# Performance work log

Hardware: AMD Instinct MI355X
Metric: run time of the kernel (lower is better)

Reference implementation:

```python
import jax, jax.numpy as jnp
import numpy as np

N_NODES = 50000
N_EDGES = 800000
IN_CH, HID_CH, OUT_CH = 256, 128, 64


def setup_inputs() -> dict:
    key = jax.random.key(0)
    k_x, k_e, k_w1, k_w2 = jax.random.split(key, 4)
    x = jax.random.normal(k_x, (N_NODES, IN_CH), dtype=jnp.float32)
    edge_index = jax.random.randint(k_e, (2, N_EDGES), 0, N_NODES, dtype=jnp.int32)
    # Glorot-style init like PyG GCNConv (weight [in, out], bias zeros)
    s1 = float(np.sqrt(6.0 / (IN_CH + HID_CH)))
    s2 = float(np.sqrt(6.0 / (HID_CH + OUT_CH)))
    W1 = jax.random.uniform(k_w1, (IN_CH, HID_CH), jnp.float32, -s1, s1)
    b1 = jnp.zeros((HID_CH,), jnp.float32)
    W2 = jax.random.uniform(k_w2, (HID_CH, OUT_CH), jnp.float32, -s2, s2)
    b2 = jnp.zeros((OUT_CH,), jnp.float32)
    return {"x": x, "edge_index": edge_index, "W1": W1, "b1": b1, "W2": W2, "b2": b2}


def _gcn_conv(x, src, dst, deg_inv_sqrt, W, b, n_nodes):
    """GCNConv with self-loops: D^{-1/2}(A+I)D^{-1/2} X W + b."""
    h = x @ W  # [N, out]
    norm = deg_inv_sqrt[src] * deg_inv_sqrt[dst]          # [E]
    msgs = h[src] * norm[:, None]                          # [E, out] gather
    agg = jax.ops.segment_sum(msgs, dst, num_segments=n_nodes)  # scatter-add
    self_loop = h * (deg_inv_sqrt * deg_inv_sqrt)[:, None]      # self-loop term
    return agg + self_loop + b


def reference(x, edge_index, W1, b1, W2, b2):
    n = x.shape[0]
    src, dst = edge_index[0], edge_index[1]
    # degree includes self-loop (+1), edge weight 1, counted at destination
    deg = jnp.zeros((n,), x.dtype).at[dst].add(1.0) + 1.0
    dis = jax.lax.rsqrt(deg)
    h = jax.nn.relu(_gcn_conv(x, src, dst, dis, W1, b1, n))
    out = jax.nn.relu(_gcn_conv(h, src, dst, dis, W2, b2, n))
    return out
```

## Files before the change

### kernel.cpp

```cpp
#include <hip/hip_runtime.h>

#define N_NODES 50000
#define N_EDGES 800000
#define IN_CH 256
#define HID_CH 128
#define OUT_CH 64
#define CAP 64
#define NBINS 196
#define PCHUNK 3200
#define PBLOCKS 250
#define SWZ_ELEMS (IN_CH * HID_CH + HID_CH * OUT_CH)
#define SWZ_BLOCKS (SWZ_ELEMS / 256)

typedef _Float16 f16;
typedef _Float16 f16x8 __attribute__((ext_vector_type(8)));
typedef float f32x4 __attribute__((ext_vector_type(4)));
typedef unsigned short u16;
typedef unsigned int u32;

template <int K, int N>
__device__ __forceinline__ void swz(const float* __restrict__ W, f16* __restrict__ Bsw,
                                    int idx) {
    constexpr int NTILES = N / 16;
    int j = idx & 7;
    int lane = (idx >> 3) & 63;
    int rest = idx >> 9;
    int nt = rest % NTILES;
    int ks = rest / NTILES;
    int k = ks * 32 + (lane >> 4) * 8 + j;
    int n = nt * 16 + (lane & 15);
    Bsw[idx] = (f16)W[(size_t)k * N + n];
}

__device__ __forceinline__ void scan_local(const int* __restrict__ binCnt,
                                           int* sc, int* vv) {
    const int t = threadIdx.x;
    int v = (t < NBINS) ? binCnt[t] : 0;
    sc[t] = v; vv[t] = v;
    __syncthreads();
    for (int ofs = 1; ofs < 256; ofs <<= 1) {
        int add = (t >= ofs) ? sc[t - ofs] : 0;
        __syncthreads();
        sc[t] += add;
        __syncthreads();
    }
}

__global__ __launch_bounds__(256) void k_pre(const int* __restrict__ dst,
                                             int* __restrict__ binCnt,
                                             const float* __restrict__ W1,
                                             const float* __restrict__ W2,
                                             f16* __restrict__ B1,
                                             f16* __restrict__ B2) {
    if ((int)blockIdx.x < PBLOCKS) {
        __shared__ int lcnt[NBINS];
        for (int i = threadIdx.x; i < NBINS; i += 256) lcnt[i] = 0;
        __syncthreads();
        int base = blockIdx.x * PCHUNK;
        for (int i = base + (int)threadIdx.x; i < base + PCHUNK; i += 256)
            atomicAdd(&lcnt[dst[i] >> 8], 1);
        __syncthreads();
        for (int i = threadIdx.x; i < NBINS; i += 256)
            if (lcnt[i]) atomicAdd(&binCnt[i], lcnt[i]);
        return;
    }
    int idx = ((int)blockIdx.x - PBLOCKS) * 256 + threadIdx.x;
    if (idx < IN_CH * HID_CH) {
        swz<IN_CH, HID_CH>(W1, B1, idx);
    } else {
        idx -= IN_CH * HID_CH;
        if (idx < HID_CH * OUT_CH) swz<HID_CH, OUT_CH>(W2, B2, idx);
    }
}

__global__ __launch_bounds__(256) void k_place(const int* __restrict__ src,
                                               const int* __restrict__ dst,
                                               const int* __restrict__ binCnt,
                                               int* __restrict__ binCursor,
                                               u32* __restrict__ ebuf, int E) {
    __shared__ u32 codes[PCHUNK];
    __shared__ int sc[256], vv[256];
    __shared__ int lcnt[NBINS], lbase[NBINS], lcur[NBINS];
    scan_local(binCnt, sc, vv);
    for (int i = threadIdx.x; i < NBINS; i += 256) lcnt[i] = 0;
    __syncthreads();
    int base = blockIdx.x * PCHUNK;
    int m = min(PCHUNK, E - base);
    for (int j = threadIdx.x; j < m; j += 256) {
        u32 d = (u32)dst[base + j];
        codes[j] = (d << 16) | (u32)src[base + j];
        atomicAdd(&lcnt[d >> 8], 1);
    }
    __syncthreads();
    for (int i = threadIdx.x; i < NBINS; i += 256) {
        lbase[i] = (sc[i] - vv[i]) + atomicAdd(&binCursor[i], lcnt[i]);
        lcur[i] = 0;
    }
    __syncthreads();
    for (int j = threadIdx.x; j < m; j += 256) {
        u32 c = codes[j];
        int b = c >> 24;
        int p = atomicAdd(&lcur[b], 1);
        ebuf[lbase[b] + p] = c;
    }
}

__global__ __launch_bounds__(256) void k_build(const u32* __restrict__ ebuf,
                                               const int* __restrict__ binCnt,
                                               int* __restrict__ cnt,
                                               float* __restrict__ dis,
                                               u16* __restrict__ bucket, int N) {
    __shared__ int sc[256], vv[256];
    __shared__ int lcnt[256];
    __shared__ u16 lbuck[256 * CAP];
    scan_local(binCnt, sc, vv);
    int t = threadIdx.x;
    lcnt[t] = 0;
    __syncthreads();
    int b = blockIdx.x;
    int s = sc[b] - vv[b];
    int e = sc[b];
    for (int i = s + t; i < e; i += 256) {
        u32 c = ebuf[i];
        int local = (c >> 16) & 255;
        int p = atomicAdd(&lcnt[local], 1);
        if (p < CAP) lbuck[local * CAP + p] = (u16)(c & 0xFFFFu);
    }
    __syncthreads();
    int nodeBase = b << 8;
    if (nodeBase + t < N) {
        cnt[nodeBase + t] = lcnt[t];
        dis[nodeBase + t] = rsqrtf((float)lcnt[t] + 1.0f);
    }
    const uint4* lsrc = (const uint4*)lbuck;
    uint4* gdst = (uint4*)(bucket + (size_t)nodeBase * CAP);
    for (int idx = t; idx < 256 * CAP / 8; idx += 256) {
        int row = idx >> 3;
        int chunk = idx & 7;
        if (nodeBase + row < N && (chunk << 3) < lcnt[row]) gdst[idx] = lsrc[idx];
    }
}

template <int K, int N, bool A_FP32, bool RELU>
__global__ __launch_bounds__(256) void k_gemm(const void* __restrict__ Av,
                                              const f16* __restrict__ Bsw,
                                              const float* __restrict__ dis,
                                              f16* __restrict__ C, int M) {
    constexpr int KSTEPS = K / 32, NTILES = N / 16;
    const int tid = threadIdx.x;
    const int wave = tid >> 6, lane = tid & 63;
    const int quad = lane >> 4, l16 = lane & 15;
    int row = blockIdx.x * 64 + wave * 16 + l16;
    const int rowc = row < M ? row : M - 1;

    f32x4 acc[NTILES];
#pragma unroll
    for (int t = 0; t < NTILES; ++t) acc[t] = (f32x4){0.f, 0.f, 0.f, 0.f};

#pragma unroll
    for (int ks = 0; ks < KSTEPS; ++ks) {
        f16x8 afrag;
        if (A_FP32) {
            const float* A = (const float*)Av;
            const float4* p = (const float4*)(A + (size_t)rowc * K + ks * 32 + quad * 8);
            float4 v0 = p[0], v1 = p[1];
            afrag[0] = (f16)v0.x; afrag[1] = (f16)v0.y;
            afrag[2] = (f16)v0.z; afrag[3] = (f16)v0.w;
            afrag[4] = (f16)v1.x; afrag[5] = (f16)v1.y;
            afrag[6] = (f16)v1.z; afrag[7] = (f16)v1.w;
        } else {
            const f16* A = (const f16*)Av;
            afrag = *(const f16x8*)(A + (size_t)rowc * K + ks * 32 + quad * 8);
            if (RELU) {
#pragma unroll
                for (int j = 0; j < 8; ++j)
                    afrag[j] = afrag[j] > (f16)0 ? afrag[j] : (f16)0;
            }
        }
#pragma unroll
        for (int t = 0; t < NTILES; ++t) {
            f16x8 bfrag = *(const f16x8*)(Bsw + (((size_t)ks * NTILES + t) * 64 + lane) * 8);
            acc[t] = __builtin_amdgcn_mfma_f32_16x16x32_f16(afrag, bfrag, acc[t], 0, 0, 0);
        }
    }

    int rbase = blockIdx.x * 64 + wave * 16 + quad * 4;
#pragma unroll
    for (int r = 0; r < 4; ++r) {
        int gr = rbase + r;
        if (gr < M) {
            float d = dis[gr];
#pragma unroll
            for (int t = 0; t < NTILES; ++t)
                C[(size_t)gr * N + t * 16 + l16] = (f16)(acc[t][r] * d);
        }
    }
}

__global__ __launch_bounds__(256) void k_pullgemm(const f16* __restrict__ g1,
                                                  const float* __restrict__ dis,
                                                  const float* __restrict__ b1,
                                                  const int* __restrict__ cnt,
                                                  const u16* __restrict__ bucket,
                                                  const f16* __restrict__ B2sw,
                                                  f16* __restrict__ g2) {
    constexpr int LDSW = HID_CH + 8;
    __shared__ f16 aggl[64 * LDSW];
    const int tid = threadIdx.x;
    const int sub = tid & 15;
    const int nl = tid >> 4;
    const int blockBase = (int)blockIdx.x * 64;

    const float4* b1p = (const float4*)(b1 + sub * 8);
    float4 bb0 = b1p[0], bb1 = b1p[1];
    float bv[8] = {bb0.x, bb0.y, bb0.z, bb0.w, bb1.x, bb1.y, bb1.z, bb1.w};

    for (int it = 0; it < 4; ++it) {
        int lrow = it * 16 + nl;
        int u = blockBase + lrow;
        f16x8 o;
        if (u < N_NODES) {
            const f16* gp = g1 + sub * 8;
            f16x8 sv = *(const f16x8*)(gp + (size_t)u * HID_CH);
            float a[8];
#pragma unroll
            for (int j = 0; j < 8; ++j) a[j] = (float)sv[j];

            int n = cnt[u];
            if (n > CAP) n = CAP;
            const u16* row = bucket + u * CAP;

            int k = 0;
            for (; k + 8 <= n; k += 8) {
                uint4 iv = *(const uint4*)(row + k);
                int s0 = iv.x & 0xFFFF, s1 = iv.x >> 16;
                int s2 = iv.y & 0xFFFF, s3 = iv.y >> 16;
                int s4 = iv.z & 0xFFFF, s5 = iv.z >> 16;
                int s6 = iv.w & 0xFFFF, s7 = iv.w >> 16;
                f16x8 v0 = *(const f16x8*)(gp + (size_t)s0 * HID_CH);
                f16x8 v1 = *(const f16x8*)(gp + (size_t)s1 * HID_CH);
                f16x8 v2 = *(const f16x8*)(gp + (size_t)s2 * HID_CH);
                f16x8 v3 = *(const f16x8*)(gp + (size_t)s3 * HID_CH);
                f16x8 v4 = *(const f16x8*)(gp + (size_t)s4 * HID_CH);
                f16x8 v5 = *(const f16x8*)(gp + (size_t)s5 * HID_CH);
                f16x8 v6 = *(const f16x8*)(gp + (size_t)s6 * HID_CH);
                f16x8 v7 = *(const f16x8*)(gp + (size_t)s7 * HID_CH);
#pragma unroll
                for (int j = 0; j < 8; ++j)
                    a[j] += (((float)v0[j] + (float)v1[j]) + ((float)v2[j] + (float)v3[j])) +
                            (((float)v4[j] + (float)v5[j]) + ((float)v6[j] + (float)v7[j]));
            }
            if (k + 4 <= n) {
                ushort4 s4v = *(const ushort4*)(row + k);
                f16x8 v0 = *(const f16x8*)(gp + (size_t)s4v.x * HID_CH);
                f16x8 v1 = *(const f16x8*)(gp + (size_t)s4v.y * HID_CH);
                f16x8 v2 = *(const f16x8*)(gp + (size_t)s4v.z * HID_CH);
                f16x8 v3 = *(const f16x8*)(gp + (size_t)s4v.w * HID_CH);
#pragma unroll
                for (int j = 0; j < 8; ++j)
                    a[j] += ((float)v0[j] + (float)v1[j]) + ((float)v2[j] + (float)v3[j]);
                k += 4;
            }
            for (; k < n; ++k) {
                f16x8 v = *(const f16x8*)(gp + (size_t)row[k] * HID_CH);
#pragma unroll
                for (int j = 0; j < 8; ++j) a[j] += (float)v[j];
            }

            float du = dis[u];
#pragma unroll
            for (int j = 0; j < 8; ++j) {
                float t = fmaf(du, a[j], bv[j]);
                o[j] = (f16)(t > 0.f ? t : 0.f);
            }
        } else {
#pragma unroll
            for (int j = 0; j < 8; ++j) o[j] = (f16)0;
        }
        *(f16x8*)(aggl + (size_t)lrow * LDSW + sub * 8) = o;
    }
    __syncthreads();

    constexpr int KSTEPS = HID_CH / 32, NTILES = OUT_CH / 16;
    const int wave = tid >> 6, lane = tid & 63;
    const int quad = lane >> 4, l16 = lane & 15;
    const int lrowA = wave * 16 + l16;

    f32x4 acc[NTILES];
#pragma unroll
    for (int t = 0; t < NTILES; ++t) acc[t] = (f32x4){0.f, 0.f, 0.f, 0.f};

#pragma unroll
    for (int ks = 0; ks < KSTEPS; ++ks) {
        f16x8 afrag = *(const f16x8*)(aggl + (size_t)lrowA * LDSW + ks * 32 + quad * 8);
#pragma unroll
        for (int t = 0; t < NTILES; ++t) {
            f16x8 bfrag = *(const f16x8*)(B2sw + (((size_t)ks * NTILES + t) * 64 + lane) * 8);
            acc[t] = __builtin_amdgcn_mfma_f32_16x16x32_f16(afrag, bfrag, acc[t], 0, 0, 0);
        }
    }

    int rbase = blockBase + wave * 16 + quad * 4;
#pragma unroll
    for (int r = 0; r < 4; ++r) {
        int gr = rbase + r;
        if (gr < N_NODES) {
            float d = dis[gr];
#pragma unroll
            for (int t = 0; t < NTILES; ++t)
                g2[(size_t)gr * OUT_CH + t * 16 + l16] = (f16)(acc[t][r] * d);
        }
    }
}

__global__ __launch_bounds__(256) void k_pull2(const f16* __restrict__ g2,
                                               const float* __restrict__ dis,
                                               const float* __restrict__ b2,
                                               const int* __restrict__ cnt,
                                               const u16* __restrict__ bucket,
                                               float* __restrict__ out) {
    int gtid = blockIdx.x * 256 + threadIdx.x;
    int u = gtid >> 3;
    int sub = gtid & 7;
    if (u >= N_NODES) return;
    const f16* gp = g2 + sub * 8;

    f16x8 sv = *(const f16x8*)(gp + (size_t)u * OUT_CH);
    float a[8];
#pragma unroll
    for (int j = 0; j < 8; ++j) a[j] = (float)sv[j];

    int n = cnt[u];
    if (n > CAP) n = CAP;
    const u16* row = bucket + u * CAP;

    int k = 0;
    for (; k + 8 <= n; k += 8) {
        uint4 iv = *(const uint4*)(row + k);
        int s0 = iv.x & 0xFFFF, s1 = iv.x >> 16;
        int s2 = iv.y & 0xFFFF, s3 = iv.y >> 16;
        int s4 = iv.z & 0xFFFF, s5 = iv.z >> 16;
        int s6 = iv.w & 0xFFFF, s7 = iv.w >> 16;
        f16x8 v0 = *(const f16x8*)(gp + (size_t)s0 * OUT_CH);
        f16x8 v1 = *(const f16x8*)(gp + (size_t)s1 * OUT_CH);
        f16x8 v2 = *(const f16x8*)(gp + (size_t)s2 * OUT_CH);
        f16x8 v3 = *(const f16x8*)(gp + (size_t)s3 * OUT_CH);
        f16x8 v4 = *(const f16x8*)(gp + (size_t)s4 * OUT_CH);
        f16x8 v5 = *(const f16x8*)(gp + (size_t)s5 * OUT_CH);
        f16x8 v6 = *(const f16x8*)(gp + (size_t)s6 * OUT_CH);
        f16x8 v7 = *(const f16x8*)(gp + (size_t)s7 * OUT_CH);
#pragma unroll
        for (int j = 0; j < 8; ++j)
            a[j] += (((float)v0[j] + (float)v1[j]) + ((float)v2[j] + (float)v3[j])) +
                    (((float)v4[j] + (float)v5[j]) + ((float)v6[j] + (float)v7[j]));
    }
    if (k + 4 <= n) {
        ushort4 s4v = *(const ushort4*)(row + k);
        f16x8 v0 = *(const f16x8*)(gp + (size_t)s4v.x * OUT_CH);
        f16x8 v1 = *(const f16x8*)(gp + (size_t)s4v.y * OUT_CH);
        f16x8 v2 = *(const f16x8*)(gp + (size_t)s4v.z * OUT_CH);
        f16x8 v3 = *(const f16x8*)(gp + (size_t)s4v.w * OUT_CH);
#pragma unroll
        for (int j = 0; j < 8; ++j)
            a[j] += ((float)v0[j] + (float)v1[j]) + ((float)v2[j] + (float)v3[j]);
        k += 4;
    }
    for (; k < n; ++k) {
        f16x8 v = *(const f16x8*)(gp + (size_t)row[k] * OUT_CH);
#pragma unroll
        for (int j = 0; j < 8; ++j) a[j] += (float)v[j];
    }

    float du = dis[u];
    float4* op = (float4*)(out + (size_t)u * OUT_CH + sub * 8);
    float4 o0, o1;
    o0.x = fmaxf(fmaf(du, a[0], b2[sub * 8 + 0]), 0.f);
    o0.y = fmaxf(fmaf(du, a[1], b2[sub * 8 + 1]), 0.f);
    o0.z = fmaxf(fmaf(du, a[2], b2[sub * 8 + 2]), 0.f);
    o0.w = fmaxf(fmaf(du, a[3], b2[sub * 8 + 3]), 0.f);
    o1.x = fmaxf(fmaf(du, a[4], b2[sub * 8 + 4]), 0.f);
    o1.y = fmaxf(fmaf(du, a[5], b2[sub * 8 + 5]), 0.f);
    o1.z = fmaxf(fmaf(du, a[6], b2[sub * 8 + 6]), 0.f);
    o1.w = fmaxf(fmaf(du, a[7], b2[sub * 8 + 7]), 0.f);
    op[0] = o0;
    op[1] = o1;
}


extern "C" void kernel_launch(void* const* d_in, const int* in_sizes, int n_in,
                              void* d_out, int out_size, void* d_ws, size_t ws_size,
                              hipStream_t stream) {
    const float* x  = (const float*)d_in[0];
    const int* ei   = (const int*)d_in[1];
    const float* W1 = (const float*)d_in[2];
    const float* b1 = (const float*)d_in[3];
    const float* W2 = (const float*)d_in[4];
    const float* b2 = (const float*)d_in[5];
    float* out = (float*)d_out;

    const int* src = ei;
    const int* dst = ei + N_EDGES;

    char* ws = (char*)d_ws;
    size_t off = 0;
    auto alloc = [&](size_t bytes) -> void* {
        off = (off + 255) & ~(size_t)255;
        void* p = ws + off;
        off += bytes;
        return p;
    };
    int*   zbuf      = (int*)alloc((size_t)(NBINS * 2) * 4);
    int*   binCnt    = zbuf;
    int*   binCursor = zbuf + NBINS;
    u32*   ebuf      = (u32*)alloc((size_t)N_EDGES * 4);
    int*   cnt       = (int*)alloc((size_t)N_NODES * 4);
    float* dis       = (float*)alloc((size_t)N_NODES * 4);
    u16*   bucket    = (u16*)alloc((size_t)N_NODES * CAP * 2);
    f16*   W1sw      = (f16*)alloc((size_t)IN_CH * HID_CH * 2);
    f16*   W2sw      = (f16*)alloc((size_t)HID_CH * OUT_CH * 2);
    f16*   g1        = (f16*)alloc((size_t)N_NODES * HID_CH * 2);
    f16*   g2        = (f16*)alloc((size_t)N_NODES * OUT_CH * 2);

    hipMemsetAsync(zbuf, 0, (size_t)(NBINS * 2) * 4, stream);

    k_pre<<<PBLOCKS + SWZ_BLOCKS, 256, 0, stream>>>(dst, binCnt, W1, W2, W1sw, W2sw);
    k_place<<<PBLOCKS, 256, 0, stream>>>(src, dst, binCnt, binCursor, ebuf, N_EDGES);
    k_build<<<NBINS, 256, 0, stream>>>(ebuf, binCnt, cnt, dis, bucket, N_NODES);

    k_gemm<IN_CH, HID_CH, true, false><<<(N_NODES + 63) / 64, 256, 0, stream>>>(
        x, W1sw, dis, g1, N_NODES);

    k_pullgemm<<<(N_NODES + 63) / 64, 256, 0, stream>>>(g1, dis, b1, cnt, bucket,
                                                        W2sw, g2);

    k_pull2<<<(N_NODES * 8 + 255) / 256, 256, 0, stream>>>(g2, dis, b2, cnt, bucket, out);
}
```

Baseline: 198.5 us.

## Widen parallelism in bucket build, edge placement and pull-GEMM aggregation

Splits each k_build bin across two blocks, so each block handles 128 nodes and uses half the shared memory. It also halves the edge chunk per placement block, doubling the block count. k_pullgemm now launches 1024 threads per block, so each of 64 nodes is gathered by its own 16 threads in one pass instead of four sequential passes. Only the first 256 threads then run the MFMA GEMM. The aim is more memory-level parallelism in the latency-bound gather and placement phases, at the cost of each k_build block re-reading its whole bin and idle threads during the GEMM step.

```diff
diff --git a/kernel.cpp b/kernel.cpp
--- a/kernel.cpp
+++ b/kernel.cpp
@@ -7,8 +7,8 @@
 #define OUT_CH 64
 #define CAP 64
 #define NBINS 196
-#define PCHUNK 3200
-#define PBLOCKS 250
+#define PCHUNK 1600
+#define PBLOCKS 500
 #define SWZ_ELEMS (IN_CH * HID_CH + HID_CH * OUT_CH)
 #define SWZ_BLOCKS (SWZ_ELEMS / 256)
 
@@ -111,41 +111,45 @@
                                                float* __restrict__ dis,
                                                u16* __restrict__ bucket, int N) {
     __shared__ int sc[256], vv[256];
-    __shared__ int lcnt[256];
-    __shared__ u16 lbuck[256 * CAP];
+    __shared__ int lcnt[128];
+    __shared__ u16 lbuck[128 * CAP];
     scan_local(binCnt, sc, vv);
     int t = threadIdx.x;
-    lcnt[t] = 0;
-    __syncthreads();
-    int b = blockIdx.x;
+    if (t < 128) lcnt[t] = 0;
+    __syncthreads();
+    int b = blockIdx.x >> 1;
+    int half = blockIdx.x & 1;
     int s = sc[b] - vv[b];
     int e = sc[b];
     for (int i = s + t; i < e; i += 256) {
         u32 c = ebuf[i];
         int local = (c >> 16) & 255;
-        int p = atomicAdd(&lcnt[local], 1);
-        if (p < CAP) lbuck[local * CAP + p] = (u16)(c & 0xFFFFu);
-    }
-    __syncthreads();
-    int nodeBase = b << 8;
-    if (nodeBase + t < N) {
+        if ((local >> 7) == half) {
+            int l = local & 127;
+            int p = atomicAdd(&lcnt[l], 1);
+            if (p < CAP) lbuck[l * CAP + p] = (u16)(c & 0xFFFFu);
+        }
+    }
+    __syncthreads();
+    int nodeBase = (b << 8) + (half << 7);
+    if (t < 128 && nodeBase + t < N) {
         cnt[nodeBase + t] = lcnt[t];
         dis[nodeBase + t] = rsqrtf((float)lcnt[t] + 1.0f);
     }
     const uint4* lsrc = (const uint4*)lbuck;
     uint4* gdst = (uint4*)(bucket + (size_t)nodeBase * CAP);
-    for (int idx = t; idx < 256 * CAP / 8; idx += 256) {
+    for (int idx = t; idx < 128 * CAP / 8; idx += 256) {
         int row = idx >> 3;
         int chunk = idx & 7;
         if (nodeBase + row < N && (chunk << 3) < lcnt[row]) gdst[idx] = lsrc[idx];
     }
 }
 
-template <int K, int N, bool A_FP32, bool RELU>
-__global__ __launch_bounds__(256) void k_gemm(const void* __restrict__ Av,
-                                              const f16* __restrict__ Bsw,
-                                              const float* __restrict__ dis,
-                                              f16* __restrict__ C, int M) {
+__global__ __launch_bounds__(256) void k_gemm1(const float* __restrict__ A,
+                                               const f16* __restrict__ Bsw,
+                                               const float* __restrict__ dis,
+                                               f16* __restrict__ C, int M) {
+    constexpr int K = IN_CH, N = HID_CH;
     constexpr int KSTEPS = K / 32, NTILES = N / 16;
     const int tid = threadIdx.x;
     const int wave = tid >> 6, lane = tid & 63;
@@ -160,23 +164,12 @@
 #pragma unroll
     for (int ks = 0; ks < KSTEPS; ++ks) {
         f16x8 afrag;
-        if (A_FP32) {
-            const float* A = (const float*)Av;
-            const float4* p = (const float4*)(A + (size_t)rowc * K + ks * 32 + quad * 8);
-            float4 v0 = p[0], v1 = p[1];
-            afrag[0] = (f16)v0.x; afrag[1] = (f16)v0.y;
-            afrag[2] = (f16)v0.z; afrag[3] = (f16)v0.w;
-            afrag[4] = (f16)v1.x; afrag[5] = (f16)v1.y;
-            afrag[6] = (f16)v1.z; afrag[7] = (f16)v1.w;
-        } else {
-            const f16* A = (const f16*)Av;
-            afrag = *(const f16x8*)(A + (size_t)rowc * K + ks * 32 + quad * 8);
-            if (RELU) {
-#pragma unroll
-                for (int j = 0; j < 8; ++j)
-                    afrag[j] = afrag[j] > (f16)0 ? afrag[j] : (f16)0;
-            }
-        }
+        const float4* p = (const float4*)(A + (size_t)rowc * K + ks * 32 + quad * 8);
+        float4 v0 = p[0], v1 = p[1];
+        afrag[0] = (f16)v0.x; afrag[1] = (f16)v0.y;
+        afrag[2] = (f16)v0.z; afrag[3] = (f16)v0.w;
+        afrag[4] = (f16)v1.x; afrag[5] = (f16)v1.y;
+        afrag[6] = (f16)v1.z; afrag[7] = (f16)v1.w;
 #pragma unroll
         for (int t = 0; t < NTILES; ++t) {
             f16x8 bfrag = *(const f16x8*)(Bsw + (((size_t)ks * NTILES + t) * 64 + lane) * 8);
@@ -197,118 +190,116 @@
     }
 }
 
-__global__ __launch_bounds__(256) void k_pullgemm(const f16* __restrict__ g1,
-                                                  const float* __restrict__ dis,
-                                                  const float* __restrict__ b1,
-                                                  const int* __restrict__ cnt,
-                                                  const u16* __restrict__ bucket,
-                                                  const f16* __restrict__ B2sw,
-                                                  f16* __restrict__ g2) {
+__global__ __launch_bounds__(1024, 8) void k_pullgemm(const f16* __restrict__ g1,
+                                                      const float* __restrict__ dis,
+                                                      const float* __restrict__ b1,
+                                                      const int* __restrict__ cnt,
+                                                      const u16* __restrict__ bucket,
+                                                      const f16* __restrict__ B2sw,
+                                                      f16* __restrict__ g2) {
     constexpr int LDSW = HID_CH + 8;
     __shared__ f16 aggl[64 * LDSW];
     const int tid = threadIdx.x;
     const int sub = tid & 15;
     const int nl = tid >> 4;
     const int blockBase = (int)blockIdx.x * 64;
-
-    const float4* b1p = (const float4*)(b1 + sub * 8);
-    float4 bb0 = b1p[0], bb1 = b1p[1];
-    float bv[8] = {bb0.x, bb0.y, bb0.z, bb0.w, bb1.x, bb1.y, bb1.z, bb1.w};
-
-    for (int it = 0; it < 4; ++it) {
-        int lrow = it * 16 + nl;
-        int u = blockBase + lrow;
-        f16x8 o;
-        if (u < N_NODES) {
-            const f16* gp = g1 + sub * 8;
-            f16x8 sv = *(const f16x8*)(gp + (size_t)u * HID_CH);
-            float a[8];
-#pragma unroll
-            for (int j = 0; j < 8; ++j) a[j] = (float)sv[j];
-
-            int n = cnt[u];
-            if (n > CAP) n = CAP;
-            const u16* row = bucket + u * CAP;
-
-            int k = 0;
-            for (; k + 8 <= n; k += 8) {
-                uint4 iv = *(const uint4*)(row + k);
-                int s0 = iv.x & 0xFFFF, s1 = iv.x >> 16;
-                int s2 = iv.y & 0xFFFF, s3 = iv.y >> 16;
-                int s4 = iv.z & 0xFFFF, s5 = iv.z >> 16;
-                int s6 = iv.w & 0xFFFF, s7 = iv.w >> 16;
-                f16x8 v0 = *(const f16x8*)(gp + (size_t)s0 * HID_CH);
-                f16x8 v1 = *(const f16x8*)(gp + (size_t)s1 * HID_CH);
-                f16x8 v2 = *(const f16x8*)(gp + (size_t)s2 * HID_CH);
-                f16x8 v3 = *(const f16x8*)(gp + (size_t)s3 * HID_CH);
-                f16x8 v4 = *(const f16x8*)(gp + (size_t)s4 * HID_CH);
-                f16x8 v5 = *(const f16x8*)(gp + (size_t)s5 * HID_CH);
-                f16x8 v6 = *(const f16x8*)(gp + (size_t)s6 * HID_CH);
-                f16x8 v7 = *(const f16x8*)(gp + (size_t)s7 * HID_CH);
-#pragma unroll
-                for (int j = 0; j < 8; ++j)
-                    a[j] += (((float)v0[j] + (float)v1[j]) + ((float)v2[j] + (float)v3[j])) +
-                            (((float)v4[j] + (float)v5[j]) + ((float)v6[j] + (float)v7[j]));
+    const int u = blockBase + nl;
+
+    f16x8 o;
+    if (u < N_NODES) {
+        const f16* gp = g1 + sub * 8;
+        f16x8 sv = *(const f16x8*)(gp + (size_t)u * HID_CH);
+        float a[8];
+#pragma unroll
+        for (int j = 0; j < 8; ++j) a[j] = (float)sv[j];
+
+        int n = cnt[u];
+        if (n > CAP) n = CAP;
+        const u16* row = bucket + u * CAP;
+
+        int k = 0;
+        for (; k + 8 <= n; k += 8) {
+            uint4 iv = *(const uint4*)(row + k);
+            int s0 = iv.x & 0xFFFF, s1 = iv.x >> 16;
+            int s2 = iv.y & 0xFFFF, s3 = iv.y >> 16;
+            int s4 = iv.z & 0xFFFF, s5 = iv.z >> 16;
+            int s6 = iv.w & 0xFFFF, s7 = iv.w >> 16;
+            f16x8 v0 = *(const f16x8*)(gp + (size_t)s0 * HID_CH);
+            f16x8 v1 = *(const f16x8*)(gp + (size_t)s1 * HID_CH);
+            f16x8 v2 = *(const f16x8*)(gp + (size_t)s2 * HID_CH);
+            f16x8 v3 = *(const f16x8*)(gp + (size_t)s3 * HID_CH);
+            f16x8 v4 = *(const f16x8*)(gp + (size_t)s4 * HID_CH);
+            f16x8 v5 = *(const f16x8*)(gp + (size_t)s5 * HID_CH);
+            f16x8 v6 = *(const f16x8*)(gp + (size_t)s6 * HID_CH);
+            f16x8 v7 = *(const f16x8*)(gp + (size_t)s7 * HID_CH);
+#pragma unroll
+            for (int j = 0; j < 8; ++j)
+                a[j] += (((float)v0[j] + (float)v1[j]) + ((float)v2[j] + (float)v3[j])) +
+                        (((float)v4[j] + (float)v5[j]) + ((float)v6[j] + (float)v7[j]));
+        }
+        if (k + 4 <= n) {
+            ushort4 s4v = *(const ushort4*)(row + k);
+            f16x8 v0 = *(const f16x8*)(gp + (size_t)s4v.x * HID_CH);
+            f16x8 v1 = *(const f16x8*)(gp + (size_t)s4v.y * HID_CH);
+            f16x8 v2 = *(const f16x8*)(gp + (size_t)s4v.z * HID_CH);
+            f16x8 v3 = *(const f16x8*)(gp + (size_t)s4v.w * HID_CH);
+#pragma unroll
+            for (int j = 0; j < 8; ++j)
+                a[j] += ((float)v0[j] + (float)v1[j]) + ((float)v2[j] + (float)v3[j]);
+            k += 4;
+        }
+        for (; k < n; ++k) {
+            f16x8 v = *(const f16x8*)(gp + (size_t)row[k] * HID_CH);
+#pragma unroll
+            for (int j = 0; j < 8; ++j) a[j] += (float)v[j];
+        }
+
+        float du = dis[u];
+        const float4* b1p = (const float4*)(b1 + sub * 8);
+        float4 bb0 = b1p[0], bb1 = b1p[1];
+        float bv[8] = {bb0.x, bb0.y, bb0.z, bb0.w, bb1.x, bb1.y, bb1.z, bb1.w};
+#pragma unroll
+        for (int j = 0; j < 8; ++j) {
+            float t = fmaf(du, a[j], bv[j]);
+            o[j] = (f16)(t > 0.f ? t : 0.f);
+        }
+    } else {
+#pragma unroll
+        for (int j = 0; j < 8; ++j) o[j] = (f16)0;
+    }
+    *(f16x8*)(aggl + (size_t)nl * LDSW + sub * 8) = o;
+    __syncthreads();
+
+    if (tid < 256) {
+        constexpr int KSTEPS = HID_CH / 32, NTILES = OUT_CH / 16;
+        const int wave = tid >> 6, lane = tid & 63;
+        const int quad = lane >> 4, l16 = lane & 15;
+        const int lrowA = wave * 16 + l16;
+
+        f32x4 acc[NTILES];
+#pragma unroll
+        for (int t = 0; t < NTILES; ++t) acc[t] = (f32x4){0.f, 0.f, 0.f, 0.f};
+
+#pragma unroll
+        for (int ks = 0; ks < KSTEPS; ++ks) {
+            f16x8 afrag = *(const f16x8*)(aggl + (size_t)lrowA * LDSW + ks * 32 + quad * 8);
+#pragma unroll
+            for (int t = 0; t < NTILES; ++t) {
+                f16x8 bfrag = *(const f16x8*)(B2sw + (((size_t)ks * NTILES + t) * 64 + lane) * 8);
+                acc[t] = __builtin_amdgcn_mfma_f32_16x16x32_f16(afrag, bfrag, acc[t], 0, 0, 0);
             }
-            if (k + 4 <= n) {
-                ushort4 s4v = *(const ushort4*)(row + k);
-                f16x8 v0 = *(const f16x8*)(gp + (size_t)s4v.x * HID_CH);
-                f16x8 v1 = *(const f16x8*)(gp + (size_t)s4v.y * HID_CH);
-                f16x8 v2 = *(const f16x8*)(gp + (size_t)s4v.z * HID_CH);
-                f16x8 v3 = *(const f16x8*)(gp + (size_t)s4v.w * HID_CH);
-#pragma unroll
-                for (int j = 0; j < 8; ++j)
-                    a[j] += ((float)v0[j] + (float)v1[j]) + ((float)v2[j] + (float)v3[j]);
-                k += 4;
+        }
+
+        int rbase = blockBase + wave * 16 + quad * 4;
+#pragma unroll
+        for (int r = 0; r < 4; ++r) {
+            int gr = rbase + r;
+            if (gr < N_NODES) {
+                float d = dis[gr];
+#pragma unroll
+                for (int t = 0; t < NTILES; ++t)
+                    g2[(size_t)gr * OUT_CH + t * 16 + l16] = (f16)(acc[t][r] * d);
             }
-            for (; k < n; ++k) {
-                f16x8 v = *(const f16x8*)(gp + (size_t)row[k] * HID_CH);
-#pragma unroll
-                for (int j = 0; j < 8; ++j) a[j] += (float)v[j];
-            }
-
-            float du = dis[u];
-#pragma unroll
-            for (int j = 0; j < 8; ++j) {
-                float t = fmaf(du, a[j], bv[j]);
-                o[j] = (f16)(t > 0.f ? t : 0.f);
-            }
-        } else {
-#pragma unroll
-            for (int j = 0; j < 8; ++j) o[j] = (f16)0;
-        }
-        *(f16x8*)(aggl + (size_t)lrow * LDSW + sub * 8) = o;
-    }
-    __syncthreads();
-
-    constexpr int KSTEPS = HID_CH / 32, NTILES = OUT_CH / 16;
-    const int wave = tid >> 6, lane = tid & 63;
-    const int quad = lane >> 4, l16 = lane & 15;
-    const int lrowA = wave * 16 + l16;
-
-    f32x4 acc[NTILES];
-#pragma unroll
-    for (int t = 0; t < NTILES; ++t) acc[t] = (f32x4){0.f, 0.f, 0.f, 0.f};
-
-#pragma unroll
-    for (int ks = 0; ks < KSTEPS; ++ks) {
-        f16x8 afrag = *(const f16x8*)(aggl + (size_t)lrowA * LDSW + ks * 32 + quad * 8);
-#pragma unroll
-        for (int t = 0; t < NTILES; ++t) {
-            f16x8 bfrag = *(const f16x8*)(B2sw + (((size_t)ks * NTILES + t) * 64 + lane) * 8);
-            acc[t] = __builtin_amdgcn_mfma_f32_16x16x32_f16(afrag, bfrag, acc[t], 0, 0, 0);
-        }
-    }
-
-    int rbase = blockBase + wave * 16 + quad * 4;
-#pragma unroll
-    for (int r = 0; r < 4; ++r) {
-        int gr = rbase + r;
-        if (gr < N_NODES) {
-            float d = dis[gr];
-#pragma unroll
-            for (int t = 0; t < NTILES; ++t)
-                g2[(size_t)gr * OUT_CH + t * 16 + l16] = (f16)(acc[t][r] * d);
         }
     }
 }
@@ -425,13 +416,12 @@
 
     k_pre<<<PBLOCKS + SWZ_BLOCKS, 256, 0, stream>>>(dst, binCnt, W1, W2, W1sw, W2sw);
     k_place<<<PBLOCKS, 256, 0, stream>>>(src, dst, binCnt, binCursor, ebuf, N_EDGES);
-    k_build<<<NBINS, 256, 0, stream>>>(ebuf, binCnt, cnt, dis, bucket, N_NODES);
-
-    k_gemm<IN_CH, HID_CH, true, false><<<(N_NODES + 63) / 64, 256, 0, stream>>>(
-        x, W1sw, dis, g1, N_NODES);
-
-    k_pullgemm<<<(N_NODES + 63) / 64, 256, 0, stream>>>(g1, dis, b1, cnt, bucket,
-                                                        W2sw, g2);
+    k_build<<<NBINS * 2, 256, 0, stream>>>(ebuf, binCnt, cnt, dis, bucket, N_NODES);
+
+    k_gemm1<<<(N_NODES + 63) / 64, 256, 0, stream>>>(x, W1sw, dis, g1, N_NODES);
+
+    k_pullgemm<<<(N_NODES + 63) / 64, 1024, 0, stream>>>(g1, dis, b1, cnt, bucket,
+                                                         W2sw, g2);
 
     k_pull2<<<(N_NODES * 8 + 255) / 256, 256, 0, stream>>>(g2, dis, b2, cnt, bucket, out);
 }
```

Measured after the change: 211.9 us. 6.8% more time.
